# Kernel optimization log

Hardware: AMD Instinct MI355X
Metric: run time of the kernel (lower is better)

The kernel has to match this reference:

```python
import jax, jax.numpy as jnp
import numpy as np

N_SRC0, N_DST0 = 200000, 50000
N_DST1 = 10000
D_IN, D_HID = 128, 128


def _sage_mean(h, src, dst, n_dst, W_self, b_self, W_neigh, b_neigh, act):
    # gather messages from src nodes, mean-aggregate per dst node
    msg = h[src]                                             # [E, D]
    agg = jax.ops.segment_sum(msg, dst, num_segments=n_dst)  # [n_dst, D]
    deg = jax.ops.segment_sum(jnp.ones(dst.shape, h.dtype), dst, num_segments=n_dst)
    h_neigh = agg / jnp.maximum(deg, 1.0)[:, None]
    # DGL block convention: dst nodes are the first n_dst src nodes
    rst = h[:n_dst] @ W_self + b_self + h_neigh @ W_neigh + b_neigh
    return jax.nn.relu(rst) if act else rst


def setup_inputs() -> dict:
    key = jax.random.key(0)
    ks = jax.random.split(key, 12)
    s = 1.0 / np.sqrt(D_HID)
    return {
        "features": jax.random.normal(ks[0], (N_SRC0, D_IN), jnp.float32),
        "src0": jax.random.randint(ks[1], (800000,), 0, N_SRC0),
        "dst0": jax.random.randint(ks[2], (800000,), 0, N_DST0),
        "src1": jax.random.randint(ks[3], (160000,), 0, N_DST0),
        "dst1": jax.random.randint(ks[4], (160000,), 0, N_DST1),
        "W_init": jax.random.uniform(ks[5], (D_IN, D_HID), jnp.float32, -s, s),
        "b_init": jax.random.uniform(ks[6], (D_HID,), jnp.float32, -s, s),
        "W_self": jax.random.uniform(ks[7], (D_HID, D_HID), jnp.float32, -s, s),
        "b_self": jax.random.uniform(ks[8], (D_HID,), jnp.float32, -s, s),
        "W_neigh": jax.random.uniform(ks[9], (D_HID, D_HID), jnp.float32, -s, s),
        "b_neigh": jax.random.uniform(ks[10], (D_HID,), jnp.float32, -s, s),
    }


def reference(features, src0, dst0, src1, dst1, W_init, b_init, W_self, b_self, W_neigh, b_neigh):
    # fc_init + activation
    h = jax.nn.relu(features @ W_init + b_init)              # [N_SRC0, D_HID]
    # block 0 (act_flag True), dropout p=0.0 is identity
    h = _sage_mean(h, src0, dst0, N_DST0, W_self, b_self, W_neigh, b_neigh, act=True)
    # block 1 (last block: act_flag False)
    h = _sage_mean(h, src1, dst1, N_DST1, W_self, b_self, W_neigh, b_neigh, act=False)
    return jnp.squeeze(h, axis=1) if h.shape[1] == 1 else h  # h.squeeze(1) no-op for D_HID>1
```

## Files before the change

### kernel.cpp

```cpp
#include <hip/hip_runtime.h>
#include <stdint.h>
#include <stddef.h>


#define DIM 128
constexpr int N_SRC0 = 200000;
constexpr int N_DST0 = 50000;
constexpr int N_DST1 = 10000;
constexpr int E0 = 800000;
constexpr int E1 = 160000;
constexpr int MAXDEG = 64;

typedef __attribute__((ext_vector_type(8))) short bf16x8;
typedef __attribute__((ext_vector_type(4))) float f32x4;

__device__ __forceinline__ uint16_t f2bf(float f) {
  union { float f; uint32_t u; } v; v.f = f;
  return (uint16_t)((v.u + 0x7FFFu + ((v.u >> 16) & 1u)) >> 16);
}
__device__ __forceinline__ float bf2f(uint16_t h) {
  union { uint32_t u; float f; } v; v.u = ((uint32_t)h) << 16;
  return v.f;
}

__global__ __launch_bounds__(512) void prep_w_kernel(
    const float* __restrict__ W0, const float* __restrict__ W1,
    const float* __restrict__ W2, uint16_t* __restrict__ Wf,
    int* __restrict__ cnt, int ncnt) {
  int gid = blockIdx.x * 512 + threadIdx.x;
  if (gid < 3 * 16384) {
    int m = gid >> 14, idx = gid & 16383;
    const float* W = m == 0 ? W0 : (m == 1 ? W1 : W2);
    int j = idx & 7, lane = (idx >> 3) & 63, nt = (idx >> 9) & 7, kc = idx >> 12;
    int k = kc * 32 + (lane >> 4) * 8 + j;
    int n = nt * 16 + (lane & 15);
    Wf[gid] = f2bf(W[k * DIM + n]);
  }
  int z = gid - 3 * 16384;
  if (z >= 0 && z < ncnt) cnt[z] = 0;
}

__global__ __launch_bounds__(256) void place_kernel(
    const int* __restrict__ src0, const int* __restrict__ dst0,
    const int* __restrict__ src1, const int* __restrict__ dst1,
    int* __restrict__ cnt0, int* __restrict__ cnt1,
    int* __restrict__ eslot0, int* __restrict__ eslot1) {
  int part = blockIdx.x & 7;
  int bpp  = gridDim.x >> 3;
  int bidx = blockIdx.x >> 3;
  const int4* s04 = (const int4*)src0;
  const int4* d04 = (const int4*)dst0;
  const int4* s14 = (const int4*)src1;
  const int4* d14 = (const int4*)dst1;

  int lo = part * (N_DST0 / 8), hi = lo + (N_DST0 / 8);
  for (int i = bidx * 256 + threadIdx.x; i < E0 / 4; i += bpp * 256) {
    int4 d = d04[i]; int4 s = s04[i];
    if (d.x >= lo && d.x < hi) { int p = atomicAdd(&cnt0[d.x], 1); if (p < MAXDEG) eslot0[(size_t)d.x * MAXDEG + p] = s.x; }
    if (d.y >= lo && d.y < hi) { int p = atomicAdd(&cnt0[d.y], 1); if (p < MAXDEG) eslot0[(size_t)d.y * MAXDEG + p] = s.y; }
    if (d.z >= lo && d.z < hi) { int p = atomicAdd(&cnt0[d.z], 1); if (p < MAXDEG) eslot0[(size_t)d.z * MAXDEG + p] = s.z; }
    if (d.w >= lo && d.w < hi) { int p = atomicAdd(&cnt0[d.w], 1); if (p < MAXDEG) eslot0[(size_t)d.w * MAXDEG + p] = s.w; }
  }
  int lo1 = part * (N_DST1 / 8), hi1 = lo1 + (N_DST1 / 8);
  for (int i = bidx * 256 + threadIdx.x; i < E1 / 4; i += bpp * 256) {
    int4 d = d14[i]; int4 s = s14[i];
    if (d.x >= lo1 && d.x < hi1) { int p = atomicAdd(&cnt1[d.x], 1); if (p < MAXDEG) eslot1[(size_t)d.x * MAXDEG + p] = s.x; }
    if (d.y >= lo1 && d.y < hi1) { int p = atomicAdd(&cnt1[d.y], 1); if (p < MAXDEG) eslot1[(size_t)d.y * MAXDEG + p] = s.y; }
    if (d.z >= lo1 && d.z < hi1) { int p = atomicAdd(&cnt1[d.z], 1); if (p < MAXDEG) eslot1[(size_t)d.z * MAXDEG + p] = s.z; }
    if (d.w >= lo1 && d.w < hi1) { int p = atomicAdd(&cnt1[d.w], 1); if (p < MAXDEG) eslot1[(size_t)d.w * MAXDEG + p] = s.w; }
  }
}

__global__ __launch_bounds__(256) void fc_init_kernel(
    const float* __restrict__ feat, const uint16_t* __restrict__ Wf,
    const float* __restrict__ bias, uint16_t* __restrict__ hout) {
  __shared__ uint16_t wl[16384];
  __shared__ __align__(16) float tile[2][4096];
  {
    const uint4* g = (const uint4*)Wf;
    uint4* s = (uint4*)wl;
    for (int i = threadIdx.x; i < 2048; i += 256) s[i] = g[i];
  }
  const int tid = threadIdx.x;
  const int w = tid >> 6, lane = tid & 63;
  const int q = lane >> 4, m16 = lane & 15;
  const int sl = w >> 1, nh = w & 1;

  float bv[4];
#pragma unroll
  for (int j = 0; j < 4; j++) bv[j] = bias[(nh * 4 + j) * 16 + m16];

  const int ntiles = N_SRC0 / 32;
  const int stride = gridDim.x;

  auto stage = [&](int t, int buf) {
    const float* gbase = feat + (size_t)t * 4096 + w * 1024 + lane * 4;
    float* lbase = &tile[buf][w * 1024];
#pragma unroll
    for (int i = 0; i < 4; i++) {
      __builtin_amdgcn_global_load_lds(
          (const __attribute__((address_space(1))) uint32_t*)(gbase + i * 256),
          (__attribute__((address_space(3))) uint32_t*)(lbase + i * 256),
          16, 0, 0);
    }
  };

  int t = blockIdx.x;
  int cur = 0;
  if (t < ntiles) stage(t, 0);
  __syncthreads();

  while (t < ntiles) {
    int tn = t + stride;
    if (tn < ntiles) stage(tn, cur ^ 1);

    f32x4 acc[4];
#pragma unroll
    for (int j = 0; j < 4; j++) acc[j] = (f32x4){0.f, 0.f, 0.f, 0.f};

    const float* arow = &tile[cur][(sl * 16 + m16) * 128];
#pragma unroll
    for (int kc = 0; kc < 4; kc++) {
      float4 x0 = *(const float4*)(arow + kc * 32 + q * 8);
      float4 x1 = *(const float4*)(arow + kc * 32 + q * 8 + 4);
      float xs[8] = {x0.x, x0.y, x0.z, x0.w, x1.x, x1.y, x1.z, x1.w};
      bf16x8 a;
#pragma unroll
      for (int j = 0; j < 8; j++) a[j] = (short)f2bf(xs[j]);
#pragma unroll
      for (int j = 0; j < 4; j++) {
        int nt = nh * 4 + j;
        bf16x8 wv = *(const bf16x8*)&wl[((kc * 8 + nt) * 64 + lane) * 8];
        acc[j] = __builtin_amdgcn_mfma_f32_16x16x32_bf16(a, wv, acc[j], 0, 0, 0);
      }
    }

    int rowb = t * 32 + sl * 16 + q * 4;
#pragma unroll
    for (int j = 0; j < 4; j++)
#pragma unroll
      for (int r = 0; r < 4; r++) {
        float v = fmaxf(acc[j][r] + bv[j], 0.f);
        hout[(size_t)(rowb + r) * DIM + (nh * 4 + j) * 16 + m16] = f2bf(v);
      }

    __syncthreads();
    cur ^= 1;
    t = tn;
  }
}

__global__ __launch_bounds__(256) void agg_kernel(
    const int* __restrict__ eslot, const int* __restrict__ deg,
    const uint16_t* __restrict__ hsrc, uint16_t* __restrict__ hout, int n_dst) {
  int d = (blockIdx.x * 256 + threadIdx.x) >> 6;
  int lane = threadIdx.x & 63;
  if (d >= n_dst) return;
  const int* sl = eslot + (size_t)d * MAXDEG;
  int dg = deg[d];
  int dgc = dg < MAXDEG ? dg : MAXDEG;
  float a0 = 0.f, a1 = 0.f;
  int e = 0;
  for (; e + 4 <= dgc; e += 4) {
    int s0 = sl[e], s1 = sl[e + 1], s2 = sl[e + 2], s3 = sl[e + 3];
    uint32_t p0 = *(const uint32_t*)(hsrc + (size_t)s0 * DIM + lane * 2);
    uint32_t p1 = *(const uint32_t*)(hsrc + (size_t)s1 * DIM + lane * 2);
    uint32_t p2 = *(const uint32_t*)(hsrc + (size_t)s2 * DIM + lane * 2);
    uint32_t p3 = *(const uint32_t*)(hsrc + (size_t)s3 * DIM + lane * 2);
    a0 += bf2f((uint16_t)p0) + bf2f((uint16_t)p1) + bf2f((uint16_t)p2) + bf2f((uint16_t)p3);
    a1 += bf2f((uint16_t)(p0 >> 16)) + bf2f((uint16_t)(p1 >> 16)) +
          bf2f((uint16_t)(p2 >> 16)) + bf2f((uint16_t)(p3 >> 16));
  }
  for (; e < dgc; e++) {
    uint32_t p = *(const uint32_t*)(hsrc + (size_t)sl[e] * DIM + lane * 2);
    a0 += bf2f((uint16_t)p);
    a1 += bf2f((uint16_t)(p >> 16));
  }
  float inv = 1.f / fmaxf((float)dg, 1.f);
  uint32_t o = (uint32_t)f2bf(a0 * inv) | ((uint32_t)f2bf(a1 * inv) << 16);
  *(uint32_t*)(hout + (size_t)d * DIM + lane * 2) = o;
}

template <bool ACT, bool OUT_BF16>
__global__ __launch_bounds__(256) void sage_kernel(
    const uint16_t* __restrict__ hself, const uint16_t* __restrict__ hneigh,
    const uint16_t* __restrict__ WfS, const uint16_t* __restrict__ WfN,
    const float* __restrict__ bS, const float* __restrict__ bN,
    void* __restrict__ outp, int n_dst) {
  __shared__ uint16_t wS[16384];
  __shared__ uint16_t wN[16384];
  {
    const uint4* gS = (const uint4*)WfS;
    const uint4* gN = (const uint4*)WfN;
    uint4* sS = (uint4*)wS;
    uint4* sN = (uint4*)wN;
    for (int i = threadIdx.x; i < 2048; i += 256) { sS[i] = gS[i]; sN[i] = gN[i]; }
  }
  __syncthreads();

  int wave = (blockIdx.x * 256 + threadIdx.x) >> 6;
  int nwaves = (gridDim.x * 256) >> 6;
  int lane = threadIdx.x & 63;
  int q = lane >> 4, m16 = lane & 15;

  float bv[8];
#pragma unroll
  for (int nt = 0; nt < 8; nt++)
    bv[nt] = bS[nt * 16 + m16] + bN[nt * 16 + m16];

  const int nstrips = n_dst / 16;
  int s = wave;
  bf16x8 XS[4], XN[4];
  if (s < nstrips) {
    size_t ro = (size_t)(s * 16 + m16) * DIM + q * 8;
#pragma unroll
    for (int kc = 0; kc < 4; kc++) {
      XS[kc] = *(const bf16x8*)(hself + ro + kc * 32);
      XN[kc] = *(const bf16x8*)(hneigh + ro + kc * 32);
    }
  }

  while (s < nstrips) {
    int sn = s + nwaves;
    bf16x8 YS[4], YN[4];
    if (sn < nstrips) {
      size_t ro = (size_t)(sn * 16 + m16) * DIM + q * 8;
#pragma unroll
      for (int kc = 0; kc < 4; kc++) {
        YS[kc] = *(const bf16x8*)(hself + ro + kc * 32);
        YN[kc] = *(const bf16x8*)(hneigh + ro + kc * 32);
      }
    }

    f32x4 acc[8];
#pragma unroll
    for (int nt = 0; nt < 8; nt++) acc[nt] = (f32x4){0.f, 0.f, 0.f, 0.f};

#pragma unroll
    for (int kc = 0; kc < 4; kc++) {
#pragma unroll
      for (int nt = 0; nt < 8; nt++) {
        size_t fo = (size_t)((kc * 8 + nt) * 64 + lane) * 8;
        bf16x8 ws = *(const bf16x8*)&wS[fo];
        bf16x8 wn = *(const bf16x8*)&wN[fo];
        acc[nt] = __builtin_amdgcn_mfma_f32_16x16x32_bf16(XS[kc], ws, acc[nt], 0, 0, 0);
        acc[nt] = __builtin_amdgcn_mfma_f32_16x16x32_bf16(XN[kc], wn, acc[nt], 0, 0, 0);
      }
    }

    int m0 = s * 16;
#pragma unroll
    for (int nt = 0; nt < 8; nt++)
#pragma unroll
      for (int r = 0; r < 4; r++) {
        float v = acc[nt][r] + bv[nt];
        if (ACT) v = fmaxf(v, 0.f);
        size_t o = (size_t)(m0 + q * 4 + r) * DIM + nt * 16 + m16;
        if (OUT_BF16) ((uint16_t*)outp)[o] = f2bf(v);
        else          ((float*)outp)[o] = v;
      }

#pragma unroll
    for (int i = 0; i < 4; i++) { XS[i] = YS[i]; XN[i] = YN[i]; }
    s = sn;
  }
}

extern "C" void kernel_launch(void* const* d_in, const int* in_sizes, int n_in,
                              void* d_out, int out_size, void* d_ws, size_t ws_size,
                              hipStream_t stream) {
  const float* feat   = (const float*)d_in[0];
  const int* src0     = (const int*)d_in[1];
  const int* dst0     = (const int*)d_in[2];
  const int* src1     = (const int*)d_in[3];
  const int* dst1     = (const int*)d_in[4];
  const float* W_init = (const float*)d_in[5];
  const float* b_init = (const float*)d_in[6];
  const float* W_self = (const float*)d_in[7];
  const float* b_self = (const float*)d_in[8];
  const float* W_neigh= (const float*)d_in[9];
  const float* b_neigh= (const float*)d_in[10];

  char* ws = (char*)d_ws;
  uint16_t* h     = (uint16_t*)(ws + 0);
  uint16_t* h1    = (uint16_t*)(ws + 51200000);
  uint16_t* hn    = (uint16_t*)(ws + 64000000);
  int*      cnt0  = (int*)(ws + 76800000);
  int*      cnt1  = (int*)(ws + 77000000);
  int*      eslot0= (int*)(ws + 77040000);
  int*      eslot1= (int*)(ws + 89840000);
  uint16_t* WfI   = (uint16_t*)(ws + 92400000);
  uint16_t* WfS   = WfI + 16384;
  uint16_t* WfN   = WfS + 16384;

  prep_w_kernel<<<214, 512, 0, stream>>>(W_init, W_self, W_neigh, WfI, cnt0, 60000);
  place_kernel<<<1024, 256, 0, stream>>>(src0, dst0, src1, dst1,
                                         cnt0, cnt1, eslot0, eslot1);

  fc_init_kernel<<<512, 256, 0, stream>>>(feat, WfI, b_init, h);

  agg_kernel<<<N_DST0 / 4, 256, 0, stream>>>(eslot0, cnt0, h, hn, N_DST0);
  sage_kernel<true, true><<<512, 256, 0, stream>>>(h, hn, WfS, WfN, b_self, b_neigh,
                                                   h1, N_DST0);

  agg_kernel<<<N_DST1 / 4, 256, 0, stream>>>(eslot1, cnt1, h1, hn, N_DST1);
  sage_kernel<false, false><<<160, 256, 0, stream>>>(h1, hn, WfS, WfN, b_self, b_neigh,
                                                     d_out, N_DST1);
}
```

Measured before the change: 306.1 us.

## Fuse neighbor aggregation into SAGE GEMM and build weight fragments in-kernel

Merges the mean-aggregation kernel into the SAGE MFMA kernel. Each block aggregates a 16-row strip of neighbor features into shared memory and then multiplies it by both weight matrices, which removes the global round trip for the aggregated tensor and two launches. Weight conversion to bf16 fragments now happens inside every block instead of in a separate prep kernel, and the degree counters are zeroed with a memset. The cost is redundant per-block fp32-to-bf16 weight conversion, a barrier between the gather and MMA phases, and only two column tiles of MFMA work per wave.

```diff
diff --git a/kernel.cpp b/kernel.cpp
--- a/kernel.cpp
+++ b/kernel.cpp
@@ -10,6 +10,7 @@
 constexpr int E0 = 800000;
 constexpr int E1 = 160000;
 constexpr int MAXDEG = 64;
+constexpr int HNP = 136;
 
 typedef __attribute__((ext_vector_type(8))) short bf16x8;
 typedef __attribute__((ext_vector_type(4))) float f32x4;
@@ -23,21 +24,14 @@
   return v.f;
 }
 
-__global__ __launch_bounds__(512) void prep_w_kernel(
-    const float* __restrict__ W0, const float* __restrict__ W1,
-    const float* __restrict__ W2, uint16_t* __restrict__ Wf,
-    int* __restrict__ cnt, int ncnt) {
-  int gid = blockIdx.x * 512 + threadIdx.x;
-  if (gid < 3 * 16384) {
-    int m = gid >> 14, idx = gid & 16383;
-    const float* W = m == 0 ? W0 : (m == 1 ? W1 : W2);
-    int j = idx & 7, lane = (idx >> 3) & 63, nt = (idx >> 9) & 7, kc = idx >> 12;
-    int k = kc * 32 + (lane >> 4) * 8 + j;
-    int n = nt * 16 + (lane & 15);
-    Wf[gid] = f2bf(W[k * DIM + n]);
-  }
-  int z = gid - 3 * 16384;
-  if (z >= 0 && z < ncnt) cnt[z] = 0;
+__device__ __forceinline__ void build_w_frags(const float* __restrict__ W,
+                                              uint16_t* __restrict__ frag) {
+  for (int i = threadIdx.x; i < 16384; i += 256) {
+    int k = i >> 7, n = i & 127;
+    int kc = k >> 5, q = (k >> 3) & 3, j = k & 7;
+    int nt = n >> 4, ll = n & 15;
+    frag[((kc * 8 + nt) * 64 + q * 16 + ll) * 8 + j] = f2bf(W[i]);
+  }
 }
 
 __global__ __launch_bounds__(256) void place_kernel(
@@ -72,15 +66,12 @@
 }
 
 __global__ __launch_bounds__(256) void fc_init_kernel(
-    const float* __restrict__ feat, const uint16_t* __restrict__ Wf,
+    const float* __restrict__ feat, const float* __restrict__ W,
     const float* __restrict__ bias, uint16_t* __restrict__ hout) {
   __shared__ uint16_t wl[16384];
   __shared__ __align__(16) float tile[2][4096];
-  {
-    const uint4* g = (const uint4*)Wf;
-    uint4* s = (uint4*)wl;
-    for (int i = threadIdx.x; i < 2048; i += 256) s[i] = g[i];
-  }
+  build_w_frags(W, wl);
+
   const int tid = threadIdx.x;
   const int w = tid >> 6, lane = tid & 63;
   const int q = lane >> 4, m16 = lane & 15;
@@ -150,119 +141,98 @@
   }
 }
 
-__global__ __launch_bounds__(256) void agg_kernel(
+template <bool ACT, bool OUT_BF16>
+__global__ __launch_bounds__(256) void sage_fused_kernel(
     const int* __restrict__ eslot, const int* __restrict__ deg,
-    const uint16_t* __restrict__ hsrc, uint16_t* __restrict__ hout, int n_dst) {
-  int d = (blockIdx.x * 256 + threadIdx.x) >> 6;
-  int lane = threadIdx.x & 63;
-  if (d >= n_dst) return;
-  const int* sl = eslot + (size_t)d * MAXDEG;
-  int dg = deg[d];
-  int dgc = dg < MAXDEG ? dg : MAXDEG;
-  float a0 = 0.f, a1 = 0.f;
-  int e = 0;
-  for (; e + 4 <= dgc; e += 4) {
-    int s0 = sl[e], s1 = sl[e + 1], s2 = sl[e + 2], s3 = sl[e + 3];
-    uint32_t p0 = *(const uint32_t*)(hsrc + (size_t)s0 * DIM + lane * 2);
-    uint32_t p1 = *(const uint32_t*)(hsrc + (size_t)s1 * DIM + lane * 2);
-    uint32_t p2 = *(const uint32_t*)(hsrc + (size_t)s2 * DIM + lane * 2);
-    uint32_t p3 = *(const uint32_t*)(hsrc + (size_t)s3 * DIM + lane * 2);
-    a0 += bf2f((uint16_t)p0) + bf2f((uint16_t)p1) + bf2f((uint16_t)p2) + bf2f((uint16_t)p3);
-    a1 += bf2f((uint16_t)(p0 >> 16)) + bf2f((uint16_t)(p1 >> 16)) +
-          bf2f((uint16_t)(p2 >> 16)) + bf2f((uint16_t)(p3 >> 16));
-  }
-  for (; e < dgc; e++) {
-    uint32_t p = *(const uint32_t*)(hsrc + (size_t)sl[e] * DIM + lane * 2);
-    a0 += bf2f((uint16_t)p);
-    a1 += bf2f((uint16_t)(p >> 16));
-  }
-  float inv = 1.f / fmaxf((float)dg, 1.f);
-  uint32_t o = (uint32_t)f2bf(a0 * inv) | ((uint32_t)f2bf(a1 * inv) << 16);
-  *(uint32_t*)(hout + (size_t)d * DIM + lane * 2) = o;
-}
-
-template <bool ACT, bool OUT_BF16>
-__global__ __launch_bounds__(256) void sage_kernel(
-    const uint16_t* __restrict__ hself, const uint16_t* __restrict__ hneigh,
-    const uint16_t* __restrict__ WfS, const uint16_t* __restrict__ WfN,
+    const uint16_t* __restrict__ hsrc, const uint16_t* __restrict__ hself,
+    const float* __restrict__ WS, const float* __restrict__ WN,
     const float* __restrict__ bS, const float* __restrict__ bN,
     void* __restrict__ outp, int n_dst) {
   __shared__ uint16_t wS[16384];
   __shared__ uint16_t wN[16384];
-  {
-    const uint4* gS = (const uint4*)WfS;
-    const uint4* gN = (const uint4*)WfN;
-    uint4* sS = (uint4*)wS;
-    uint4* sN = (uint4*)wN;
-    for (int i = threadIdx.x; i < 2048; i += 256) { sS[i] = gS[i]; sN[i] = gN[i]; }
-  }
+  __shared__ uint16_t hn[16 * HNP];
+  build_w_frags(WS, wS);
+  build_w_frags(WN, wN);
   __syncthreads();
 
-  int wave = (blockIdx.x * 256 + threadIdx.x) >> 6;
-  int nwaves = (gridDim.x * 256) >> 6;
-  int lane = threadIdx.x & 63;
-  int q = lane >> 4, m16 = lane & 15;
-
-  float bv[8];
-#pragma unroll
-  for (int nt = 0; nt < 8; nt++)
-    bv[nt] = bS[nt * 16 + m16] + bN[nt * 16 + m16];
-
-  const int nstrips = n_dst / 16;
-  int s = wave;
-  bf16x8 XS[4], XN[4];
-  if (s < nstrips) {
-    size_t ro = (size_t)(s * 16 + m16) * DIM + q * 8;
+  const int w = threadIdx.x >> 6, lane = threadIdx.x & 63;
+  const int q = lane >> 4, m16 = lane & 15;
+
+  float bv[2];
+#pragma unroll
+  for (int j = 0; j < 2; j++) {
+    int nt = w * 2 + j;
+    bv[j] = bS[nt * 16 + m16] + bN[nt * 16 + m16];
+  }
+
+  const int ngroups = n_dst / 16;
+  for (int g = blockIdx.x; g < ngroups; g += gridDim.x) {
+    int m0 = g * 16;
+
+#pragma unroll
+    for (int rr = 0; rr < 4; rr++) {
+      int d = m0 + w * 4 + rr;
+      const int* sl = eslot + (size_t)d * MAXDEG;
+      int dg = deg[d];
+      int dgc = dg < MAXDEG ? dg : MAXDEG;
+      float a0 = 0.f, a1 = 0.f;
+      int e = 0;
+      for (; e + 8 <= dgc; e += 8) {
+        int4 sa = *(const int4*)(sl + e);
+        int4 sb = *(const int4*)(sl + e + 4);
+        uint32_t p0 = *(const uint32_t*)(hsrc + (size_t)sa.x * DIM + lane * 2);
+        uint32_t p1 = *(const uint32_t*)(hsrc + (size_t)sa.y * DIM + lane * 2);
+        uint32_t p2 = *(const uint32_t*)(hsrc + (size_t)sa.z * DIM + lane * 2);
+        uint32_t p3 = *(const uint32_t*)(hsrc + (size_t)sa.w * DIM + lane * 2);
+        uint32_t p4 = *(const uint32_t*)(hsrc + (size_t)sb.x * DIM + lane * 2);
+        uint32_t p5 = *(const uint32_t*)(hsrc + (size_t)sb.y * DIM + lane * 2);
+        uint32_t p6 = *(const uint32_t*)(hsrc + (size_t)sb.z * DIM + lane * 2);
+        uint32_t p7 = *(const uint32_t*)(hsrc + (size_t)sb.w * DIM + lane * 2);
+        a0 += bf2f((uint16_t)p0) + bf2f((uint16_t)p1) + bf2f((uint16_t)p2) + bf2f((uint16_t)p3)
+            + bf2f((uint16_t)p4) + bf2f((uint16_t)p5) + bf2f((uint16_t)p6) + bf2f((uint16_t)p7);
+        a1 += bf2f((uint16_t)(p0 >> 16)) + bf2f((uint16_t)(p1 >> 16)) + bf2f((uint16_t)(p2 >> 16)) + bf2f((uint16_t)(p3 >> 16))
+            + bf2f((uint16_t)(p4 >> 16)) + bf2f((uint16_t)(p5 >> 16)) + bf2f((uint16_t)(p6 >> 16)) + bf2f((uint16_t)(p7 >> 16));
+      }
+      for (; e < dgc; e++) {
+        uint32_t p = *(const uint32_t*)(hsrc + (size_t)sl[e] * DIM + lane * 2);
+        a0 += bf2f((uint16_t)p);
+        a1 += bf2f((uint16_t)(p >> 16));
+      }
+      float inv = 1.f / fmaxf((float)dg, 1.f);
+      uint32_t o = (uint32_t)f2bf(a0 * inv) | ((uint32_t)f2bf(a1 * inv) << 16);
+      *(uint32_t*)&hn[(w * 4 + rr) * HNP + lane * 2] = o;
+    }
+    __syncthreads();
+
+    f32x4 acc[2];
+#pragma unroll
+    for (int j = 0; j < 2; j++) acc[j] = (f32x4){0.f, 0.f, 0.f, 0.f};
+
 #pragma unroll
     for (int kc = 0; kc < 4; kc++) {
-      XS[kc] = *(const bf16x8*)(hself + ro + kc * 32);
-      XN[kc] = *(const bf16x8*)(hneigh + ro + kc * 32);
-    }
-  }
-
-  while (s < nstrips) {
-    int sn = s + nwaves;
-    bf16x8 YS[4], YN[4];
-    if (sn < nstrips) {
-      size_t ro = (size_t)(sn * 16 + m16) * DIM + q * 8;
-#pragma unroll
-      for (int kc = 0; kc < 4; kc++) {
-        YS[kc] = *(const bf16x8*)(hself + ro + kc * 32);
-        YN[kc] = *(const bf16x8*)(hneigh + ro + kc * 32);
-      }
-    }
-
-    f32x4 acc[8];
-#pragma unroll
-    for (int nt = 0; nt < 8; nt++) acc[nt] = (f32x4){0.f, 0.f, 0.f, 0.f};
-
-#pragma unroll
-    for (int kc = 0; kc < 4; kc++) {
-#pragma unroll
-      for (int nt = 0; nt < 8; nt++) {
-        size_t fo = (size_t)((kc * 8 + nt) * 64 + lane) * 8;
-        bf16x8 ws = *(const bf16x8*)&wS[fo];
-        bf16x8 wn = *(const bf16x8*)&wN[fo];
-        acc[nt] = __builtin_amdgcn_mfma_f32_16x16x32_bf16(XS[kc], ws, acc[nt], 0, 0, 0);
-        acc[nt] = __builtin_amdgcn_mfma_f32_16x16x32_bf16(XN[kc], wn, acc[nt], 0, 0, 0);
-      }
-    }
-
-    int m0 = s * 16;
-#pragma unroll
-    for (int nt = 0; nt < 8; nt++)
+      bf16x8 aS = *(const bf16x8*)(hself + (size_t)(m0 + m16) * DIM + kc * 32 + q * 8);
+      bf16x8 aN = *(const bf16x8*)&hn[m16 * HNP + kc * 32 + q * 8];
+#pragma unroll
+      for (int j = 0; j < 2; j++) {
+        int nt = w * 2 + j;
+        bf16x8 ws = *(const bf16x8*)&wS[((kc * 8 + nt) * 64 + lane) * 8];
+        bf16x8 wn = *(const bf16x8*)&wN[((kc * 8 + nt) * 64 + lane) * 8];
+        acc[j] = __builtin_amdgcn_mfma_f32_16x16x32_bf16(aS, ws, acc[j], 0, 0, 0);
+        acc[j] = __builtin_amdgcn_mfma_f32_16x16x32_bf16(aN, wn, acc[j], 0, 0, 0);
+      }
+    }
+
+#pragma unroll
+    for (int j = 0; j < 2; j++)
 #pragma unroll
       for (int r = 0; r < 4; r++) {
-        float v = acc[nt][r] + bv[nt];
+        float v = acc[j][r] + bv[j];
         if (ACT) v = fmaxf(v, 0.f);
-        size_t o = (size_t)(m0 + q * 4 + r) * DIM + nt * 16 + m16;
+        size_t o = (size_t)(m0 + q * 4 + r) * DIM + (w * 2 + j) * 16 + m16;
         if (OUT_BF16) ((uint16_t*)outp)[o] = f2bf(v);
         else          ((float*)outp)[o] = v;
       }
-
-#pragma unroll
-    for (int i = 0; i < 4; i++) { XS[i] = YS[i]; XN[i] = YN[i]; }
-    s = sn;
+    __syncthreads();
   }
 }
 
@@ -284,26 +254,18 @@
   char* ws = (char*)d_ws;
   uint16_t* h     = (uint16_t*)(ws + 0);
   uint16_t* h1    = (uint16_t*)(ws + 51200000);
-  uint16_t* hn    = (uint16_t*)(ws + 64000000);
-  int*      cnt0  = (int*)(ws + 76800000);
-  int*      cnt1  = (int*)(ws + 77000000);
-  int*      eslot0= (int*)(ws + 77040000);
-  int*      eslot1= (int*)(ws + 89840000);
-  uint16_t* WfI   = (uint16_t*)(ws + 92400000);
-  uint16_t* WfS   = WfI + 16384;
-  uint16_t* WfN   = WfS + 16384;
-
-  prep_w_kernel<<<214, 512, 0, stream>>>(W_init, W_self, W_neigh, WfI, cnt0, 60000);
+  int*      cnt0  = (int*)(ws + 64000000);
+  int*      cnt1  = (int*)(ws + 64200000);
+  int*      eslot0= (int*)(ws + 64240000);
+  int*      eslot1= (int*)(ws + 77040000);
+
+  hipMemsetAsync(cnt0, 0, 240000, stream);
   place_kernel<<<1024, 256, 0, stream>>>(src0, dst0, src1, dst1,
                                          cnt0, cnt1, eslot0, eslot1);
-
-  fc_init_kernel<<<512, 256, 0, stream>>>(feat, WfI, b_init, h);
-
-  agg_kernel<<<N_DST0 / 4, 256, 0, stream>>>(eslot0, cnt0, h, hn, N_DST0);
-  sage_kernel<true, true><<<512, 256, 0, stream>>>(h, hn, WfS, WfN, b_self, b_neigh,
-                                                   h1, N_DST0);
-
-  agg_kernel<<<N_DST1 / 4, 256, 0, stream>>>(eslot1, cnt1, h1, hn, N_DST1);
-  sage_kernel<false, false><<<160, 256, 0, stream>>>(h1, hn, WfS, WfN, b_self, b_neigh,
-                                                     d_out, N_DST1);
-}
+  fc_init_kernel<<<512, 256, 0, stream>>>(feat, W_init, b_init, h);
+
+  sage_fused_kernel<true, true><<<512, 256, 0, stream>>>(
+      eslot0, cnt0, h, h, W_self, W_neigh, b_self, b_neigh, h1, N_DST0);
+  sage_fused_kernel<false, false><<<256, 256, 0, stream>>>(
+      eslot1, cnt1, h1, h1, W_self, W_neigh, b_self, b_neigh, d_out, N_DST1);
+}
```

After: 418.1 us. 1.37x slower.

## Replace persistent pipelined GEMM loops with one-strip-per-wave grids

Applied to the files above, without the earlier changes.

The fc_init and sage kernels drop their persistent grid-stride loops, where fc_init double-buffered feature tiles through LDS via global_load_lds and sage prefetched the next strip into registers. Each wave now handles a single 16-row strip, loading its A operands straight from global memory into registers and computing all 8 output column tiles. Grids grow to cover every strip at once. The intent is more waves in flight to hide latency and removal of the tile LDS buffer and loop sync. In exchange, every block reloads the weight matrix into LDS, which greatly increases weight-staging traffic and LDS setup work. The workspace buffers are also reordered.

```diff
diff --git a/kernel.cpp b/kernel.cpp
--- a/kernel.cpp
+++ b/kernel.cpp
@@ -75,79 +75,56 @@
     const float* __restrict__ feat, const uint16_t* __restrict__ Wf,
     const float* __restrict__ bias, uint16_t* __restrict__ hout) {
   __shared__ uint16_t wl[16384];
-  __shared__ __align__(16) float tile[2][4096];
   {
     const uint4* g = (const uint4*)Wf;
     uint4* s = (uint4*)wl;
     for (int i = threadIdx.x; i < 2048; i += 256) s[i] = g[i];
   }
-  const int tid = threadIdx.x;
-  const int w = tid >> 6, lane = tid & 63;
+  __syncthreads();
+
+  const int lane = threadIdx.x & 63;
   const int q = lane >> 4, m16 = lane & 15;
-  const int sl = w >> 1, nh = w & 1;
-
-  float bv[4];
-#pragma unroll
-  for (int j = 0; j < 4; j++) bv[j] = bias[(nh * 4 + j) * 16 + m16];
-
-  const int ntiles = N_SRC0 / 32;
-  const int stride = gridDim.x;
-
-  auto stage = [&](int t, int buf) {
-    const float* gbase = feat + (size_t)t * 4096 + w * 1024 + lane * 4;
-    float* lbase = &tile[buf][w * 1024];
-#pragma unroll
-    for (int i = 0; i < 4; i++) {
-      __builtin_amdgcn_global_load_lds(
-          (const __attribute__((address_space(1))) uint32_t*)(gbase + i * 256),
-          (__attribute__((address_space(3))) uint32_t*)(lbase + i * 256),
-          16, 0, 0);
-    }
-  };
-
-  int t = blockIdx.x;
-  int cur = 0;
-  if (t < ntiles) stage(t, 0);
-  __syncthreads();
-
-  while (t < ntiles) {
-    int tn = t + stride;
-    if (tn < ntiles) stage(tn, cur ^ 1);
-
-    f32x4 acc[4];
-#pragma unroll
-    for (int j = 0; j < 4; j++) acc[j] = (f32x4){0.f, 0.f, 0.f, 0.f};
-
-    const float* arow = &tile[cur][(sl * 16 + m16) * 128];
-#pragma unroll
-    for (int kc = 0; kc < 4; kc++) {
-      float4 x0 = *(const float4*)(arow + kc * 32 + q * 8);
-      float4 x1 = *(const float4*)(arow + kc * 32 + q * 8 + 4);
-      float xs[8] = {x0.x, x0.y, x0.z, x0.w, x1.x, x1.y, x1.z, x1.w};
-      bf16x8 a;
-#pragma unroll
-      for (int j = 0; j < 8; j++) a[j] = (short)f2bf(xs[j]);
-#pragma unroll
-      for (int j = 0; j < 4; j++) {
-        int nt = nh * 4 + j;
-        bf16x8 wv = *(const bf16x8*)&wl[((kc * 8 + nt) * 64 + lane) * 8];
-        acc[j] = __builtin_amdgcn_mfma_f32_16x16x32_bf16(a, wv, acc[j], 0, 0, 0);
-      }
-    }
-
-    int rowb = t * 32 + sl * 16 + q * 4;
-#pragma unroll
-    for (int j = 0; j < 4; j++)
-#pragma unroll
-      for (int r = 0; r < 4; r++) {
-        float v = fmaxf(acc[j][r] + bv[j], 0.f);
-        hout[(size_t)(rowb + r) * DIM + (nh * 4 + j) * 16 + m16] = f2bf(v);
-      }
-
-    __syncthreads();
-    cur ^= 1;
-    t = tn;
-  }
+  const int s = blockIdx.x * 4 + (threadIdx.x >> 6);
+  if (s >= N_SRC0 / 16) return;
+
+  const float* ap = feat + (size_t)(s * 16 + m16) * DIM + q * 8;
+  float4 X[8];
+#pragma unroll
+  for (int kc = 0; kc < 4; kc++) {
+    X[2 * kc]     = *(const float4*)(ap + kc * 32);
+    X[2 * kc + 1] = *(const float4*)(ap + kc * 32 + 4);
+  }
+
+  float bv[8];
+#pragma unroll
+  for (int nt = 0; nt < 8; nt++) bv[nt] = bias[nt * 16 + m16];
+
+  f32x4 acc[8];
+#pragma unroll
+  for (int nt = 0; nt < 8; nt++) acc[nt] = (f32x4){0.f, 0.f, 0.f, 0.f};
+
+#pragma unroll
+  for (int kc = 0; kc < 4; kc++) {
+    float xs[8] = {X[2 * kc].x, X[2 * kc].y, X[2 * kc].z, X[2 * kc].w,
+                   X[2 * kc + 1].x, X[2 * kc + 1].y, X[2 * kc + 1].z, X[2 * kc + 1].w};
+    bf16x8 a;
+#pragma unroll
+    for (int j = 0; j < 8; j++) a[j] = (short)f2bf(xs[j]);
+#pragma unroll
+    for (int nt = 0; nt < 8; nt++) {
+      bf16x8 w = *(const bf16x8*)&wl[((kc * 8 + nt) * 64 + lane) * 8];
+      acc[nt] = __builtin_amdgcn_mfma_f32_16x16x32_bf16(a, w, acc[nt], 0, 0, 0);
+    }
+  }
+
+  int m0 = s * 16;
+#pragma unroll
+  for (int nt = 0; nt < 8; nt++)
+#pragma unroll
+    for (int r = 0; r < 4; r++) {
+      float v = fmaxf(acc[nt][r] + bv[nt], 0.f);
+      hout[(size_t)(m0 + q * 4 + r) * DIM + nt * 16 + m16] = f2bf(v);
+    }
 }
 
 __global__ __launch_bounds__(256) void agg_kernel(
@@ -198,72 +175,51 @@
   }
   __syncthreads();
 
-  int wave = (blockIdx.x * 256 + threadIdx.x) >> 6;
-  int nwaves = (gridDim.x * 256) >> 6;
-  int lane = threadIdx.x & 63;
-  int q = lane >> 4, m16 = lane & 15;
+  const int lane = threadIdx.x & 63;
+  const int q = lane >> 4, m16 = lane & 15;
+  const int s = blockIdx.x * 4 + (threadIdx.x >> 6);
+  if (s >= n_dst / 16) return;
+
+  size_t ro = (size_t)(s * 16 + m16) * DIM + q * 8;
+  bf16x8 XS[4], XN[4];
+#pragma unroll
+  for (int kc = 0; kc < 4; kc++) {
+    XS[kc] = *(const bf16x8*)(hself + ro + kc * 32);
+    XN[kc] = *(const bf16x8*)(hneigh + ro + kc * 32);
+  }
 
   float bv[8];
 #pragma unroll
   for (int nt = 0; nt < 8; nt++)
     bv[nt] = bS[nt * 16 + m16] + bN[nt * 16 + m16];
 
-  const int nstrips = n_dst / 16;
-  int s = wave;
-  bf16x8 XS[4], XN[4];
-  if (s < nstrips) {
-    size_t ro = (size_t)(s * 16 + m16) * DIM + q * 8;
-#pragma unroll
-    for (int kc = 0; kc < 4; kc++) {
-      XS[kc] = *(const bf16x8*)(hself + ro + kc * 32);
-      XN[kc] = *(const bf16x8*)(hneigh + ro + kc * 32);
-    }
-  }
-
-  while (s < nstrips) {
-    int sn = s + nwaves;
-    bf16x8 YS[4], YN[4];
-    if (sn < nstrips) {
-      size_t ro = (size_t)(sn * 16 + m16) * DIM + q * 8;
-#pragma unroll
-      for (int kc = 0; kc < 4; kc++) {
-        YS[kc] = *(const bf16x8*)(hself + ro + kc * 32);
-        YN[kc] = *(const bf16x8*)(hneigh + ro + kc * 32);
-      }
-    }
-
-    f32x4 acc[8];
-#pragma unroll
-    for (int nt = 0; nt < 8; nt++) acc[nt] = (f32x4){0.f, 0.f, 0.f, 0.f};
-
-#pragma unroll
-    for (int kc = 0; kc < 4; kc++) {
-#pragma unroll
-      for (int nt = 0; nt < 8; nt++) {
-        size_t fo = (size_t)((kc * 8 + nt) * 64 + lane) * 8;
-        bf16x8 ws = *(const bf16x8*)&wS[fo];
-        bf16x8 wn = *(const bf16x8*)&wN[fo];
-        acc[nt] = __builtin_amdgcn_mfma_f32_16x16x32_bf16(XS[kc], ws, acc[nt], 0, 0, 0);
-        acc[nt] = __builtin_amdgcn_mfma_f32_16x16x32_bf16(XN[kc], wn, acc[nt], 0, 0, 0);
-      }
-    }
-
-    int m0 = s * 16;
-#pragma unroll
-    for (int nt = 0; nt < 8; nt++)
-#pragma unroll
-      for (int r = 0; r < 4; r++) {
-        float v = acc[nt][r] + bv[nt];
-        if (ACT) v = fmaxf(v, 0.f);
-        size_t o = (size_t)(m0 + q * 4 + r) * DIM + nt * 16 + m16;
-        if (OUT_BF16) ((uint16_t*)outp)[o] = f2bf(v);
-        else          ((float*)outp)[o] = v;
-      }
-
-#pragma unroll
-    for (int i = 0; i < 4; i++) { XS[i] = YS[i]; XN[i] = YN[i]; }
-    s = sn;
-  }
+  f32x4 acc[8];
+#pragma unroll
+  for (int nt = 0; nt < 8; nt++) acc[nt] = (f32x4){0.f, 0.f, 0.f, 0.f};
+
+#pragma unroll
+  for (int kc = 0; kc < 4; kc++) {
+#pragma unroll
+    for (int nt = 0; nt < 8; nt++) {
+      size_t fo = (size_t)((kc * 8 + nt) * 64 + lane) * 8;
+      bf16x8 ws = *(const bf16x8*)&wS[fo];
+      bf16x8 wn = *(const bf16x8*)&wN[fo];
+      acc[nt] = __builtin_amdgcn_mfma_f32_16x16x32_bf16(XS[kc], ws, acc[nt], 0, 0, 0);
+      acc[nt] = __builtin_amdgcn_mfma_f32_16x16x32_bf16(XN[kc], wn, acc[nt], 0, 0, 0);
+    }
+  }
+
+  int m0 = s * 16;
+#pragma unroll
+  for (int nt = 0; nt < 8; nt++)
+#pragma unroll
+    for (int r = 0; r < 4; r++) {
+      float v = acc[nt][r] + bv[nt];
+      if (ACT) v = fmaxf(v, 0.f);
+      size_t o = (size_t)(m0 + q * 4 + r) * DIM + nt * 16 + m16;
+      if (OUT_BF16) ((uint16_t*)outp)[o] = f2bf(v);
+      else          ((float*)outp)[o] = v;
+    }
 }
 
 extern "C" void kernel_launch(void* const* d_in, const int* in_sizes, int n_in,
@@ -284,11 +240,11 @@
   char* ws = (char*)d_ws;
   uint16_t* h     = (uint16_t*)(ws + 0);
   uint16_t* h1    = (uint16_t*)(ws + 51200000);
-  uint16_t* hn    = (uint16_t*)(ws + 64000000);
-  int*      cnt0  = (int*)(ws + 76800000);
-  int*      cnt1  = (int*)(ws + 77000000);
-  int*      eslot0= (int*)(ws + 77040000);
-  int*      eslot1= (int*)(ws + 89840000);
+  int*      cnt0  = (int*)(ws + 64000000);
+  int*      cnt1  = (int*)(ws + 64200000);
+  int*      eslot0= (int*)(ws + 64240000);
+  int*      eslot1= (int*)(ws + 77040000);
+  uint16_t* hn    = (uint16_t*)(ws + 79600000);
   uint16_t* WfI   = (uint16_t*)(ws + 92400000);
   uint16_t* WfS   = WfI + 16384;
   uint16_t* WfN   = WfS + 16384;
@@ -297,13 +253,13 @@
   place_kernel<<<1024, 256, 0, stream>>>(src0, dst0, src1, dst1,
                                          cnt0, cnt1, eslot0, eslot1);
 
-  fc_init_kernel<<<512, 256, 0, stream>>>(feat, WfI, b_init, h);
-
-  agg_kernel<<<N_DST0 / 4, 256, 0, stream>>>(eslot0, cnt0, h, hn, N_DST0);
-  sage_kernel<true, true><<<512, 256, 0, stream>>>(h, hn, WfS, WfN, b_self, b_neigh,
-                                                   h1, N_DST0);
-
-  agg_kernel<<<N_DST1 / 4, 256, 0, stream>>>(eslot1, cnt1, h1, hn, N_DST1);
-  sage_kernel<false, false><<<160, 256, 0, stream>>>(h1, hn, WfS, WfN, b_self, b_neigh,
-                                                     d_out, N_DST1);
-}
+  fc_init_kernel<<<3125, 256, 0, stream>>>(feat, WfI, b_init, h);
+
+  agg_kernel<<<12500, 256, 0, stream>>>(eslot0, cnt0, h, hn, N_DST0);
+  sage_kernel<true, true><<<782, 256, 0, stream>>>(h, hn, WfS, WfN,
+                                                   b_self, b_neigh, h1, N_DST0);
+
+  agg_kernel<<<2500, 256, 0, stream>>>(eslot1, cnt1, h1, hn, N_DST1);
+  sage_kernel<false, false><<<157, 256, 0, stream>>>(h1, hn, WfS, WfN,
+                                                     b_self, b_neigh, d_out, N_DST1);
+}
```

After: 309.1 us. About the same (+1.0%).
